# Optimization experiments

Measured on AMD Instinct MI355X. Metric: run time of the kernel, lower is better.

## Reference

```python
import jax, jax.numpy as jnp
import numpy as np

B, N, C = 4, 32768, 128
L, H = 16, 8
D = C // H
NB = N // L
EG_H = 16  # EDGE_GATE_HIDDEN_DIM


def setup_inputs() -> dict:
    key = jax.random.key(0)
    ks = jax.random.split(key, 16)
    inp = {}
    inp["x"] = jax.random.normal(ks[0], (B, N, C), dtype=jnp.float32)
    inp["attn_mask"] = jax.random.randint(ks[1], (B, NB, L, L), 0, 2, dtype=jnp.int32)
    inp["edge_feats"] = jax.random.normal(ks[2], (B, NB, L, L, 4), dtype=jnp.float32)
    # learned parameters
    inp["Wqkv"] = jax.random.normal(ks[3], (3 * C, C), dtype=jnp.float32) * (C ** -0.5)
    inp["bqkv"] = jnp.zeros((3 * C,), dtype=jnp.float32)
    inp["Wproj"] = jax.random.normal(ks[4], (C, C), dtype=jnp.float32) * (C ** -0.5)
    inp["bproj"] = jnp.zeros((C,), dtype=jnp.float32)
    inp["eg_w1"] = jax.random.normal(ks[5], (EG_H, 4), dtype=jnp.float32) * 0.01
    inp["eg_b1"] = jnp.zeros((EG_H,), dtype=jnp.float32)
    inp["eg_w2"] = jax.random.normal(ks[6], (H, EG_H), dtype=jnp.float32) * 0.01
    inp["eg_b2"] = jnp.zeros((H,), dtype=jnp.float32)
    inp["Wbr"] = jax.random.normal(ks[7], (H, C), dtype=jnp.float32) * 0.01
    inp["bbr"] = jnp.zeros((H,), dtype=jnp.float32)
    return inp


def reference(x, attn_mask, edge_feats, Wqkv, bqkv, Wproj, bproj,
              eg_w1, eg_b1, eg_w2, eg_b2, Wbr, bbr):
    scale = D ** -0.5
    xb = x.reshape(B, NB, L, C)
    idx = jnp.arange(L)

    # bias_physics: zero the diagonal, set channel-3 diagonal to 1
    bp = edge_feats.at[:, :, idx, idx, :].set(0.0)
    bp = bp.at[:, :, idx, idx, 3].set(1.0)

    # mask: force diagonal on for rows with no valid key
    m = attn_mask.astype(x.dtype)
    need = (m.sum(axis=-1) < 1).astype(x.dtype)            # (B,NB,L)
    m = m.at[:, :, idx, idx].set(jnp.maximum(m[:, :, idx, idx], need))

    # qkv per block
    qkv = xb @ Wqkv.T + bqkv                               # (B,NB,L,3C)
    q = qkv[..., :C].reshape(B, NB, L, H, D)
    k = qkv[..., C:2 * C].reshape(B, NB, L, H, D)
    v = qkv[..., 2 * C:].reshape(B, NB, L, H, D)

    # edge-gate MLP -> per-head linear edge weights (zeroed where masked)
    h1 = jax.nn.gelu(bp @ eg_w1.T + eg_b1, approximate=False)
    ew = h1 @ eg_w2.T + eg_b2                              # (B,NB,L,L,H)
    ew = jnp.where(m[..., None] == 0, 0.0, ew)

    # logit bias = physics channel 3, masked with -inf
    logit = jnp.where(m == 0, -jnp.inf, bp[..., 3])        # (B,NB,L,L)

    scores = jnp.einsum('bnqhd,bnkhd->bnhqk', q, k) * scale + logit[:, :, None]
    attn = jax.nn.softmax(scores, axis=-1)
    x_soft = jnp.einsum('bnhqk,bnkhd->bnqhd', attn, v)

    # linear edge-weight mixing of values
    x_mid = x_soft + jnp.einsum('bnqkh,bnkhd->bnqhd', ew, v)

    # block node (use_block_node=True): mean token per block, gated value add
    blk = xb.mean(axis=2, keepdims=True)                   # (B,NB,1,C)
    v_blk = (blk @ Wqkv.T + bqkv)[..., 2 * C:].reshape(B, NB, 1, H, D)
    g_blk = jax.nn.sigmoid(xb @ Wbr.T + bbr)               # (B,NB,L,H)
    x_mid = x_mid + g_blk[..., None] * v_blk

    out = x_mid.reshape(B, N, C) @ Wproj.T + bproj
    return out
```

## Files before the change

### kernel.cpp

```cpp
#include <hip/hip_runtime.h>
#include <hip/hip_bf16.h>
#include <math.h>

typedef __attribute__((ext_vector_type(8))) short bf16x8;
typedef __attribute__((ext_vector_type(4))) short bf16x4;
typedef __attribute__((ext_vector_type(4))) float f32x4;
typedef __attribute__((ext_vector_type(4))) unsigned short us4;
typedef __attribute__((ext_vector_type(4))) __bf16 bfv4;

#define NITER 8

static __device__ __forceinline__ unsigned short f2bf_rn(float f) {
    union { __hip_bfloat16 h; unsigned short u; } cv;
    cv.h = __float2bfloat16(f);
    return cv.u;
}
static __device__ __forceinline__ bf16x4 cvt4(f32x4 v) {
    union { bfv4 b; bf16x4 s; } u;
    u.b = __builtin_convertvector(v, bfv4);
    return u.s;
}
static __device__ __forceinline__ us4 cvt4u(f32x4 v) {
    union { bfv4 b; us4 s; } u;
    u.b = __builtin_convertvector(v, bfv4);
    return u.s;
}
static __device__ __forceinline__ float bf2f(unsigned short u) {
    union { unsigned int i; float f; } cv;
    cv.i = ((unsigned int)u) << 16;
    return cv.f;
}
static __device__ __forceinline__ f32x4 MFMA(bf16x8 a, bf16x8 b, f32x4 c) {
    return __builtin_amdgcn_mfma_f32_16x16x32_bf16(a, b, c, 0, 0, 0);
}
static __device__ __forceinline__ f32x4 MFMA16(bf16x4 a, bf16x4 b, f32x4 c) {
#if __has_builtin(__builtin_amdgcn_mfma_f32_16x16x16bf16_1k)
    return __builtin_amdgcn_mfma_f32_16x16x16bf16_1k(a, b, c, 0, 0, 0);
#elif __has_builtin(__builtin_amdgcn_mfma_f32_16x16x16_bf16)
    return __builtin_amdgcn_mfma_f32_16x16x16_bf16(a, b, c, 0, 0, 0);
#else
    f32x4 d;
    asm("v_mfma_f32_16x16x16_bf16 %0, %1, %2, %3"
        : "=v"(d) : "v"(a), "v"(b), "v"(c));
    return d;
#endif
}
static __device__ __forceinline__ float sigmoid_fast(float t) {
    return __builtin_amdgcn_rcpf(1.f + __expf(-t));
}

__global__ __launch_bounds__(256) void prep_kernel(
    const float* __restrict__ Wqkv, const float* __restrict__ Wbr,
    const float* __restrict__ Wproj,
    unsigned short* __restrict__ Wbig, unsigned short* __restrict__ Wp)
{
    int i = blockIdx.x * 256 + threadIdx.x;
    if (i < 400 * 128) {
        int n = i >> 7, k = i & 127;
        float v = (n < 384) ? Wqkv[i] : (n < 392 ? Wbr[(n - 384) * 128 + k] : 0.f);
        Wbig[i] = f2bf_rn(v);
    } else {
        int j = i - 400 * 128;
        if (j < 128 * 128) Wp[j] = f2bf_rn(Wproj[j]);
    }
}

__global__ __launch_bounds__(512) void leaf_main(
    const float* __restrict__ x, const int* __restrict__ mask,
    const float* __restrict__ edge,
    const unsigned short* __restrict__ Wbig, const unsigned short* __restrict__ Wp,
    const float* __restrict__ bqkv, const float* __restrict__ bproj,
    const float* __restrict__ eg_w1, const float* __restrict__ eg_b1,
    const float* __restrict__ eg_w2, const float* __restrict__ eg_b2,
    const float* __restrict__ bbr, float* __restrict__ out)
{
    __shared__ unsigned short xS[16 * 128];
    __shared__ unsigned short mhiS[16 * 136];
    __shared__ unsigned short ewS[8 * 256];
    __shared__ float logitS[256];

    const int tid  = threadIdx.x;
    const int lane = tid & 63;
    const int wave = tid >> 6;
    const int c15  = lane & 15;
    const int quad = lane >> 4;
    const int bid0 = blockIdx.x * NITER;
    const int t0 = wave * 2, t1 = wave * 2 + 1;

    const f32x4 bqv = *(const f32x4*)&bqkv[wave * 16 + quad * 4];
    const f32x4 bkv = *(const f32x4*)&bqkv[128 + wave * 16 + quad * 4];
    const float bq2 = bqkv[256 + wave * 16 + c15];
    const float bgate = bbr[c15 & 7];
    const float bpv = bproj[wave * 16 + c15];

    bf16x4 W1a = {0, 0, 0, 0};
    if (quad == 0) {
        const f32x4 w1 = *(const f32x4*)&eg_w1[c15 * 4];
        W1a = cvt4(w1);
    }
    bf16x4 W2a = {0, 0, 0, 0};
    if (c15 < 8) {
        const f32x4 w2 = *(const f32x4*)&eg_w2[c15 * 16 + quad * 4];
        W2a = cvt4(w2);
    }
    const f32x4 b1v = *(const f32x4*)&eg_b1[quad * 4];
    f32x4 b2v = {0.f, 0.f, 0.f, 0.f};
    if (quad < 2) b2v = *(const f32x4*)&eg_b2[quad * 4];

    const unsigned short* wbase = Wbig + c15 * 128 + quad * 8;
    bf16x8 Bq[4], Bk[4], Bv[4], Wt[4];
    {
        const unsigned short* wq = wbase + (wave * 16) * 128;
        const unsigned short* wk = wbase + ((8 + wave) * 16) * 128;
        const unsigned short* wv = wbase + ((16 + wave) * 16) * 128;
        const unsigned short* wp = Wp + (wave * 16 + c15) * 128 + quad * 8;
        #pragma unroll
        for (int kk = 0; kk < 4; ++kk) {
            Bq[kk] = *(const bf16x8*)(wq + kk * 32);
            Bk[kk] = *(const bf16x8*)(wk + kk * 32);
            Bv[kk] = *(const bf16x8*)(wv + kk * 32);
            Wt[kk] = *(const bf16x8*)(wp + kk * 32);
        }
    }
    const unsigned short* wg = wbase + 384 * 128;

    int mvA = 0, mvB = 0;
    float4 evA = make_float4(0.f, 0.f, 0.f, 0.f);
    float4 evB = make_float4(0.f, 0.f, 0.f, 0.f);
    if (quad == 0) {
        const size_t base = (size_t)bid0 * 256;
        mvA = mask[base + t0 * 16 + c15];
        mvB = mask[base + t1 * 16 + c15];
        evA = *(const float4*)&edge[(base + t0 * 16 + c15) * 4];
        evB = *(const float4*)&edge[(base + t1 * 16 + c15) * 4];
    }
    float4 xv = ((const float4*)(x + (size_t)bid0 * 2048))[tid];
    {
        int row = tid >> 5, c4 = tid & 31;
        int off = row * 128 + (((c4 >> 1) ^ (row & 7)) << 3) + ((c4 & 1) << 2);
        f32x4 vv = {xv.x, xv.y, xv.z, xv.w};
        *(us4*)&xS[off] = cvt4u(vv);
    }
    __syncthreads();

    #pragma unroll 1
    for (int it = 0; it < NITER; ++it) {
        const int bid = bid0 + it;
        const bool more = (it + 1 < NITER);

        bf16x8 Bg[4];
        #pragma unroll
        for (int kk = 0; kk < 4; ++kk) Bg[kk] = *(const bf16x8*)(wg + kk * 32);

        float4 xv_n = make_float4(0.f, 0.f, 0.f, 0.f);
        int mvA_n = 0, mvB_n = 0;
        float4 evA_n = make_float4(0.f, 0.f, 0.f, 0.f);
        float4 evB_n = make_float4(0.f, 0.f, 0.f, 0.f);
        if (more) {
            xv_n = ((const float4*)(x + (size_t)(bid + 1) * 2048))[tid];
            if (quad == 0) {
                const size_t base = (size_t)(bid + 1) * 256;
                mvA_n = mask[base + t0 * 16 + c15];
                mvB_n = mask[base + t1 * 16 + c15];
                evA_n = *(const float4*)&edge[(base + t0 * 16 + c15) * 4];
                evB_n = *(const float4*)&edge[(base + t1 * 16 + c15) * 4];
            }
        }

        #pragma unroll
        for (int tt = 0; tt < 2; ++tt) {
            const int t = tt ? t1 : t0;
            const int mvt = tt ? mvB : mvA;
            const float4 evt = tt ? evB : evA;
            bf16x4 bpB = {0, 0, 0, 0};
            float bp3 = 0.f;
            if (quad == 0) {
                const bool diag = (c15 == t);
                bp3 = diag ? 1.f : evt.w;
                f32x4 bpf = {diag ? 0.f : evt.x, diag ? 0.f : evt.y,
                             diag ? 0.f : evt.z, bp3};
                bpB = cvt4(bpf);
            }
            const unsigned long long bl = __ballot(quad == 0 && mvt != 0);
            const unsigned m16 = (unsigned)(bl & 0xFFFFull);
            const bool meff = ((m16 >> c15) & 1u) || (m16 == 0u && c15 == t);
            if (quad == 0)
                logitS[t * 16 + c15] = meff ? bp3 : -INFINITY;
            f32x4 h1 = {0.f, 0.f, 0.f, 0.f};
            h1 = MFMA16(W1a, bpB, h1);
            f32x4 gv;
            #pragma unroll
            for (int r = 0; r < 4; ++r) {
                float z = h1[r] + b1v[r];
                float u = z * z;
                float w = __builtin_fmaf(-0.0664904f, u, 0.3989423f);
                gv[r] = z * __builtin_fmaf(z, w, 0.5f);
            }
            bf16x4 hB = cvt4(gv);
            f32x4 e2 = {0.f, 0.f, 0.f, 0.f};
            e2 = MFMA16(W2a, hB, e2);
            if (quad < 2) {
                #pragma unroll
                for (int r = 0; r < 4; ++r) {
                    float ewv = e2[r] + b2v[r];
                    ewS[(quad * 4 + r) * 256 + t * 16 + c15] =
                        meff ? (unsigned short)(__float_as_uint(ewv) >> 16)
                             : (unsigned short)0;
                }
            }
        }

        bf16x8 ah[4];
        #pragma unroll
        for (int kk = 0; kk < 4; ++kk) {
            int off = c15 * 128 + (((kk * 4 + quad) ^ (c15 & 7)) << 3);
            ah[kk] = *(const bf16x8*)&xS[off];
        }

        bf16x4 qa, ka, va;
        float vblk;
        float greg[4];

        {
            f32x4 acc = {0.f, 0.f, 0.f, 0.f};
            #pragma unroll
            for (int kk = 0; kk < 4; ++kk) acc = MFMA(Bq[kk], ah[kk], acc);
            qa = cvt4(acc + bqv);
        }

        {
            f32x4 acc = {0.f, 0.f, 0.f, 0.f};
            #pragma unroll
            for (int kk = 0; kk < 4; ++kk) acc = MFMA(Bk[kk], ah[kk], acc);
            ka = cvt4(acc + bkv);
        }

        {
            f32x4 acc = {0.f, 0.f, 0.f, 0.f};
            #pragma unroll
            for (int kk = 0; kk < 4; ++kk) acc = MFMA(ah[kk], Bv[kk], acc);
            f32x4 b2 = {bq2, bq2, bq2, bq2};
            va = cvt4(acc + b2);
            float s = acc[0] + acc[1] + acc[2] + acc[3];
            s += __shfl_xor(s, 16);
            s += __shfl_xor(s, 32);
            vblk = s * 0.0625f + bq2;
        }

        {
            f32x4 acc = {0.f, 0.f, 0.f, 0.f};
            #pragma unroll
            for (int kk = 0; kk < 4; ++kk) acc = MFMA(ah[kk], Bg[kk], acc);
            const int src = (lane & 48) | wave;
            #pragma unroll
            for (int r = 0; r < 4; ++r) {
                float sg = sigmoid_fast(acc[r] + bgate);
                greg[r] = __shfl(sg, src);
            }
        }
        __syncthreads();

        if (more) {
            int row = tid >> 5, c4 = tid & 31;
            int off = row * 128 + (((c4 >> 1) ^ (row & 7)) << 3) + ((c4 & 1) << 2);
            f32x4 vv = {xv_n.x, xv_n.y, xv_n.z, xv_n.w};
            *(us4*)&xS[off] = cvt4u(vv);
        }

        {
            f32x4 sc = {0.f, 0.f, 0.f, 0.f};
            sc = MFMA16(ka, qa, sc);
            const f32x4 lg = *(const f32x4*)&logitS[c15 * 16 + quad * 4];
            const us4 ew4 = *(const us4*)&ewS[wave * 256 + c15 * 16 + quad * 4];
            float e0 = __expf(__builtin_fmaf(sc[0], 0.25f, lg[0]));
            float e1 = __expf(__builtin_fmaf(sc[1], 0.25f, lg[1]));
            float e2 = __expf(__builtin_fmaf(sc[2], 0.25f, lg[2]));
            float e3 = __expf(__builtin_fmaf(sc[3], 0.25f, lg[3]));
            float sm = (e0 + e1) + (e2 + e3);
            sm += __shfl_xor(sm, 16);
            sm += __shfl_xor(sm, 32);
            const float inv = __builtin_amdgcn_rcpf(sm);
            f32x4 pv;
            pv[0] = __builtin_fmaf(e0, inv, bf2f(ew4[0]));
            pv[1] = __builtin_fmaf(e1, inv, bf2f(ew4[1]));
            pv[2] = __builtin_fmaf(e2, inv, bf2f(ew4[2]));
            pv[3] = __builtin_fmaf(e3, inv, bf2f(ew4[3]));
            bf16x4 pa = cvt4(pv);
            f32x4 xs = {0.f, 0.f, 0.f, 0.f};
            xs = MFMA16(pa, va, xs);
            f32x4 valv;
            #pragma unroll
            for (int r = 0; r < 4; ++r)
                valv[r] = xs[r] + greg[r] * vblk;
            us4 mm = cvt4u(valv);
            #pragma unroll
            for (int r = 0; r < 4; ++r) {
                const int tok = quad * 4 + r;
                mhiS[tok * 136 + wave * 16 + c15] = mm[r];
            }
        }
        __syncthreads();

        {
            bf16x8 mh[4];
            #pragma unroll
            for (int kk = 0; kk < 4; ++kk)
                mh[kk] = *(const bf16x8*)&mhiS[c15 * 136 + kk * 32 + quad * 8];
            f32x4 acc = {0.f, 0.f, 0.f, 0.f};
            #pragma unroll
            for (int kk = 0; kk < 4; ++kk) acc = MFMA(mh[kk], Wt[kk], acc);
            float* op = out + (size_t)bid * 2048;
            #pragma unroll
            for (int r = 0; r < 4; ++r)
                op[(quad * 4 + r) * 128 + wave * 16 + c15] = acc[r] + bpv;
        }

        mvA = mvA_n; mvB = mvB_n;
        evA = evA_n; evB = evB_n;
    }
}

extern "C" void kernel_launch(void* const* d_in, const int* in_sizes, int n_in,
                              void* d_out, int out_size, void* d_ws, size_t ws_size,
                              hipStream_t stream) {
    const float* x     = (const float*)d_in[0];
    const int*   amask = (const int*)  d_in[1];
    const float* edge  = (const float*)d_in[2];
    const float* Wqkv  = (const float*)d_in[3];
    const float* bqkv  = (const float*)d_in[4];
    const float* Wproj = (const float*)d_in[5];
    const float* bproj = (const float*)d_in[6];
    const float* eg_w1 = (const float*)d_in[7];
    const float* eg_b1 = (const float*)d_in[8];
    const float* eg_w2 = (const float*)d_in[9];
    const float* eg_b2 = (const float*)d_in[10];
    const float* Wbr   = (const float*)d_in[11];
    const float* bbr   = (const float*)d_in[12];
    float* outp = (float*)d_out;

    unsigned short* Wbig = (unsigned short*)d_ws;
    unsigned short* Wp   = (unsigned short*)((char*)d_ws + 400 * 128 * 2);

    hipLaunchKernelGGL(prep_kernel, dim3(264), dim3(256), 0, stream,
                       Wqkv, Wbr, Wproj, Wbig, Wp);
    hipLaunchKernelGGL(leaf_main, dim3(8192 / NITER), dim3(512), 0, stream,
                       x, amask, edge, Wbig, Wp, bqkv, bproj,
                       eg_w1, eg_b1, eg_w2, eg_b2, bbr, outp);
}
```

Before: 84.87 us.

## Transpose MFMA outputs for vectorized stores and compute gate once per block

```diff
diff --git a/kernel.cpp b/kernel.cpp
--- a/kernel.cpp
+++ b/kernel.cpp
@@ -78,6 +78,8 @@
     __shared__ unsigned short mhiS[16 * 136];
     __shared__ unsigned short ewS[8 * 256];
     __shared__ float logitS[256];
+    __shared__ float gST[128];
+    __shared__ float vbS[128];
 
     const int tid  = threadIdx.x;
     const int lane = tid & 63;
@@ -91,7 +93,7 @@
     const f32x4 bkv = *(const f32x4*)&bqkv[128 + wave * 16 + quad * 4];
     const float bq2 = bqkv[256 + wave * 16 + c15];
     const float bgate = bbr[c15 & 7];
-    const float bpv = bproj[wave * 16 + c15];
+    const f32x4 bpv4 = *(const f32x4*)&bproj[wave * 16 + quad * 4];
 
     bf16x4 W1a = {0, 0, 0, 0};
     if (quad == 0) {
@@ -149,8 +151,10 @@
         const bool more = (it + 1 < NITER);
 
         bf16x8 Bg[4];
-        #pragma unroll
-        for (int kk = 0; kk < 4; ++kk) Bg[kk] = *(const bf16x8*)(wg + kk * 32);
+        if (wave == 0) {
+            #pragma unroll
+            for (int kk = 0; kk < 4; ++kk) Bg[kk] = *(const bf16x8*)(wg + kk * 32);
+        }
 
         float4 xv_n = make_float4(0.f, 0.f, 0.f, 0.f);
         int mvA_n = 0, mvB_n = 0;
@@ -218,8 +222,6 @@
         }
 
         bf16x4 qa, ka, va;
-        float vblk;
-        float greg[4];
 
         {
             f32x4 acc = {0.f, 0.f, 0.f, 0.f};
@@ -244,18 +246,17 @@
             float s = acc[0] + acc[1] + acc[2] + acc[3];
             s += __shfl_xor(s, 16);
             s += __shfl_xor(s, 32);
-            vblk = s * 0.0625f + bq2;
-        }
-
-        {
+            if (lane < 16) vbS[wave * 16 + c15] = s * 0.0625f + bq2;
+        }
+
+        if (wave == 0) {
             f32x4 acc = {0.f, 0.f, 0.f, 0.f};
             #pragma unroll
             for (int kk = 0; kk < 4; ++kk) acc = MFMA(ah[kk], Bg[kk], acc);
-            const int src = (lane & 48) | wave;
-            #pragma unroll
-            for (int r = 0; r < 4; ++r) {
-                float sg = sigmoid_fast(acc[r] + bgate);
-                greg[r] = __shfl(sg, src);
+            if (c15 < 8) {
+                #pragma unroll
+                for (int r = 0; r < 4; ++r)
+                    gST[c15 * 16 + quad * 4 + r] = sigmoid_fast(acc[r] + bgate);
             }
         }
         __syncthreads();
@@ -287,17 +288,14 @@
             pv[3] = __builtin_fmaf(e3, inv, bf2f(ew4[3]));
             bf16x4 pa = cvt4(pv);
             f32x4 xs = {0.f, 0.f, 0.f, 0.f};
-            xs = MFMA16(pa, va, xs);
+            xs = MFMA16(va, pa, xs);
+            const float g = gST[wave * 16 + c15];
+            const f32x4 vb4 = *(const f32x4*)&vbS[wave * 16 + quad * 4];
             f32x4 valv;
             #pragma unroll
             for (int r = 0; r < 4; ++r)
-                valv[r] = xs[r] + greg[r] * vblk;
-            us4 mm = cvt4u(valv);
-            #pragma unroll
-            for (int r = 0; r < 4; ++r) {
-                const int tok = quad * 4 + r;
-                mhiS[tok * 136 + wave * 16 + c15] = mm[r];
-            }
+                valv[r] = __builtin_fmaf(g, vb4[r], xs[r]);
+            *(us4*)&mhiS[c15 * 136 + wave * 16 + quad * 4] = cvt4u(valv);
         }
         __syncthreads();
 
@@ -308,11 +306,9 @@
                 mh[kk] = *(const bf16x8*)&mhiS[c15 * 136 + kk * 32 + quad * 8];
             f32x4 acc = {0.f, 0.f, 0.f, 0.f};
             #pragma unroll
-            for (int kk = 0; kk < 4; ++kk) acc = MFMA(mh[kk], Wt[kk], acc);
+            for (int kk = 0; kk < 4; ++kk) acc = MFMA(Wt[kk], mh[kk], acc);
             float* op = out + (size_t)bid * 2048;
-            #pragma unroll
-            for (int r = 0; r < 4; ++r)
-                op[(quad * 4 + r) * 128 + wave * 16 + c15] = acc[r] + bpv;
+            *(f32x4*)&op[c15 * 128 + wave * 16 + quad * 4] = acc + bpv4;
         }
 
         mvA = mvA_n; mvB = mvB_n;
```

New measurement: 87.48 us. 1.03x slower.
